# Kernel optimization log

Hardware: AMD Instinct MI355X
Metric: run time of the kernel (lower is better)

The kernel has to match this reference:

```python
import jax, jax.numpy as jnp
import numpy as np

N, M, D = 8192, 8192, 512
TINY = jnp.finfo(jnp.float32).tiny


def setup_inputs() -> dict:
    key = jax.random.key(0)
    k1, k2 = jax.random.split(key)
    x = jax.random.normal(k1, (N, D), dtype=jnp.float32)
    x2 = jax.random.normal(k2, (M, D), dtype=jnp.float32)
    # flax self.param with ones initializer (pre-softplus raw params)
    amplitude_raw = jnp.ones((1,), dtype=jnp.float32)
    length_scale_raw = jnp.ones((D,), dtype=jnp.float32)
    return {"x": x, "x2": x2, "amplitude_raw": amplitude_raw,
            "length_scale_raw": length_scale_raw}


def reference(x, x2, amplitude_raw, length_scale_raw):
    # Parameter transforms exactly as in RBFKernelProvider.apply
    amplitude = jax.nn.softplus(amplitude_raw) + TINY          # (1,)
    length_scale = jax.nn.softplus(length_scale_raw) + TINY    # (D,)

    # rbf_kernel_fun: exp(-0.5 * sum(((x - x2)/l)^2)) * amp^2
    # GEMM rewrite of the squared scaled distance (avoids (N,M,D) intermediate):
    # ||xs_i - ys_j||^2 = ||xs_i||^2 + ||ys_j||^2 - 2 xs_i . ys_j
    xs = x / length_scale                                       # (N, D)
    ys = x2 / length_scale                                      # (M, D)
    x_sq = jnp.sum(xs * xs, axis=-1)                            # (N,)
    y_sq = jnp.sum(ys * ys, axis=-1)                            # (M,)
    cross = jnp.einsum('nd,md->nm', xs, ys)                     # (N, M) GEMM
    sq_dists = jnp.maximum(x_sq[:, None] + y_sq[None, :] - 2.0 * cross, 0.0)
    kernel_matrix = jnp.exp(-0.5 * sq_dists)                    # (N, M)
    return (amplitude ** 2) * kernel_matrix
```

## Files before the change

kernel.cpp:

```cpp
#include <hip/hip_runtime.h>

#define AS1 __attribute__((address_space(1)))
#define AS3 __attribute__((address_space(3)))

typedef __attribute__((ext_vector_type(4))) float f32x4;
typedef __attribute__((ext_vector_type(8))) int   i32x8;

static constexpr int Nn = 8192;
static constexpr int Mm = 8192;
static constexpr int Dd = 512;
static constexpr float TINY = 1.17549435082228751e-38f;

__device__ __forceinline__ float softplus_f(float x) {
    return fmaxf(x, 0.0f) + log1pf(expf(-fabsf(x)));
}

__device__ __forceinline__ float fast_exp2(float x) {
#if __has_builtin(__builtin_amdgcn_exp2f)
    return __builtin_amdgcn_exp2f(x);
#else
    return exp2f(x);
#endif
}

__device__ __forceinline__ void g2l16(const void* g, void* l) {
    __builtin_amdgcn_global_load_lds((const AS1 unsigned int*)g,
                                     (AS3 unsigned int*)l, 16, 0, 0);
}

__global__ __launch_bounds__(256) void scale_rows(
        const float* __restrict__ x, const float* __restrict__ x2,
        const float* __restrict__ ls_raw,
        unsigned char* __restrict__ xs, unsigned char* __restrict__ ys,
        float* __restrict__ x_sq, float* __restrict__ y_sq) {
    int wave = threadIdx.x >> 6, lane = threadIdx.x & 63;
    int row = blockIdx.x * 4 + wave;

    const float* src; unsigned char* dst; float* nrm; int r;
    if (row < Nn) {
        src = x  + (size_t)row * Dd; dst = xs + (size_t)row * 512;
        nrm = x_sq + row; r = row;
    } else {
        int m = row - Nn;
        src = x2 + (size_t)m * Dd;   dst = ys + (size_t)m * 512;
        nrm = y_sq + m; r = m;
    }

    float4 v0 = ((const float4*)src)[lane * 2];
    float4 v1 = ((const float4*)src)[lane * 2 + 1];
    float4 L0 = ((const float4*)ls_raw)[lane * 2];
    float4 L1 = ((const float4*)ls_raw)[lane * 2 + 1];

    float il[8] = {
        1.0f / (softplus_f(L0.x) + TINY), 1.0f / (softplus_f(L0.y) + TINY),
        1.0f / (softplus_f(L0.z) + TINY), 1.0f / (softplus_f(L0.w) + TINY),
        1.0f / (softplus_f(L1.x) + TINY), 1.0f / (softplus_f(L1.y) + TINY),
        1.0f / (softplus_f(L1.z) + TINY), 1.0f / (softplus_f(L1.w) + TINY) };
    float s[8] = { v0.x*il[0], v0.y*il[1], v0.z*il[2], v0.w*il[3],
                   v1.x*il[4], v1.y*il[5], v1.z*il[6], v1.w*il[7] };
    float sum = 0.0f;
#pragma unroll
    for (int i = 0; i < 8; ++i) sum += s[i] * s[i];

    int p0 = __builtin_amdgcn_cvt_pk_fp8_f32(s[0], s[1], 0, false);
    p0     = __builtin_amdgcn_cvt_pk_fp8_f32(s[2], s[3], p0, true);
    int p1 = __builtin_amdgcn_cvt_pk_fp8_f32(s[4], s[5], 0, false);
    p1     = __builtin_amdgcn_cvt_pk_fp8_f32(s[6], s[7], p1, true);

    int j    = lane >> 1;
    int phys = (j & ~7) | ((j & 7) ^ (r & 7));
    *(int2*)(dst + phys * 16 + (lane & 1) * 8) = make_int2(p0, p1);

#pragma unroll
    for (int off = 32; off > 0; off >>= 1) sum += __shfl_down(sum, off, 64);
    if (lane == 0) *nrm = sum;
}

__global__ __launch_bounds__(256) void gemm_rbf(
        const unsigned char* __restrict__ xs,
        const unsigned char* __restrict__ ys,
        const float* __restrict__ x_sq, const float* __restrict__ y_sq,
        const float* __restrict__ amp_raw, float* __restrict__ out) {

    __shared__ unsigned char smem[32768];
    unsigned char* sA = smem;
    unsigned char* sB = smem + 16384;
    float* sT = (float*)smem;

    const int tid  = threadIdx.x;
    const int wave = tid >> 6, lane = tid & 63;
    const int wy = wave >> 1, wx = wave & 1;
    const int lane15 = lane & 15, quad = lane >> 4;
    const int srow = lane >> 3, schunk = lane & 7;

    const unsigned lin = blockIdx.y * 64u + blockIdx.x;
    const unsigned swz = (lin & 7u) * 512u + (lin >> 3);
    const size_t rowBase = (size_t)(swz >> 6) * 128;
    const size_t colBase = (size_t)(swz & 63u) * 128;

    float xq[4][4], yq[4];
#pragma unroll
    for (int ty = 0; ty < 4; ++ty) {
        const size_t r0 = rowBase + wy * 64 + ty * 16 + quad * 4;
#pragma unroll
        for (int i = 0; i < 4; ++i) xq[ty][i] = x_sq[r0 + i];
    }
#pragma unroll
    for (int tx = 0; tx < 4; ++tx)
        yq[tx] = y_sq[colBase + wx * 64 + tx * 16 + lane15];
    float a = softplus_f(amp_raw[0]) + TINY;

    f32x4 acc[4][4] = {};

    for (int kt = 0; kt < 4; ++kt) {
        __syncthreads();
        const size_t kOff = (size_t)kt * 128;
#pragma unroll
        for (int t = 0; t < 4; ++t) {
            int issue = wave * 4 + t;
            int rit = issue * 8 + srow;
            g2l16(xs + (rowBase + rit) * 512 + kOff + schunk * 16,
                  sA + issue * 1024);
            g2l16(ys + (colBase + rit) * 512 + kOff + schunk * 16,
                  sB + issue * 1024);
        }
        __syncthreads();

        i32x8 bF[4];
#pragma unroll
        for (int tx = 0; tx < 4; ++tx) {
            int rr = wx * 64 + tx * 16 + lane15;
            int x7 = rr & 7;
            int p0 = (quad * 2 + 0) ^ x7, p1 = (quad * 2 + 1) ^ x7;
            int4 lo = *(const int4*)(sB + rr * 128 + p0 * 16);
            int4 hi = *(const int4*)(sB + rr * 128 + p1 * 16);
            i32x8 f; f[0]=lo.x; f[1]=lo.y; f[2]=lo.z; f[3]=lo.w;
                     f[4]=hi.x; f[5]=hi.y; f[6]=hi.z; f[7]=hi.w;
            bF[tx] = f;
        }
#pragma unroll
        for (int ty = 0; ty < 4; ++ty) {
            int rr = wy * 64 + ty * 16 + lane15;
            int x7 = rr & 7;
            int p0 = (quad * 2 + 0) ^ x7, p1 = (quad * 2 + 1) ^ x7;
            int4 lo = *(const int4*)(sA + rr * 128 + p0 * 16);
            int4 hi = *(const int4*)(sA + rr * 128 + p1 * 16);
            i32x8 aF; aF[0]=lo.x; aF[1]=lo.y; aF[2]=lo.z; aF[3]=lo.w;
                      aF[4]=hi.x; aF[5]=hi.y; aF[6]=hi.z; aF[7]=hi.w;
#pragma unroll
            for (int tx = 0; tx < 4; ++tx)
                acc[ty][tx] = __builtin_amdgcn_mfma_scale_f32_16x16x128_f8f6f4(
                    aF, bF[tx], acc[ty][tx],
                    0 , 0 ,
                    0, 0x7F7F7F7F,
                    0, 0x7F7F7F7F);
        }
    }

    const float L2E = 1.44269504088896340736f;
    const float la  = 2.0f * __log2f(a);
    float hx[4][4], hy[4];
#pragma unroll
    for (int ty = 0; ty < 4; ++ty)
#pragma unroll
        for (int i = 0; i < 4; ++i) hx[ty][i] = -0.5f * L2E * xq[ty][i];
#pragma unroll
    for (int tx = 0; tx < 4; ++tx) hy[tx] = -0.5f * L2E * yq[tx];

    __syncthreads();
#pragma unroll
    for (int ty = 0; ty < 4; ++ty) {
#pragma unroll
        for (int tx = 0; tx < 4; ++tx) {
#pragma unroll
            for (int reg = 0; reg < 4; ++reg) {
                float t = fminf(fmaf(acc[ty][tx][reg], L2E,
                                     hx[ty][reg] + hy[tx]), 0.0f);
                sT[(wy * 16 + quad * 4 + reg) * 132 +
                   (wx * 64 + tx * 16 + lane15)] = fast_exp2(t + la);
            }
        }
        __syncthreads();
#pragma unroll
        for (int i = 0; i < 4; ++i) {
            int l    = wave * 8 + i * 2 + (lane >> 5);
            int grow = (l >> 4) * 64 + ty * 16 + (l & 15);
            int col  = (lane & 31) * 4;
            f32x4 v  = *(const f32x4*)(sT + l * 132 + col);
            __builtin_nontemporal_store(v,
                (f32x4*)(out + (rowBase + grow) * (size_t)Mm + colBase + col));
        }
        __syncthreads();
    }
}

__global__ __launch_bounds__(256) void rbf_fallback(
        const float* __restrict__ x, const float* __restrict__ x2,
        const float* __restrict__ amp_raw, const float* __restrict__ ls_raw,
        float* __restrict__ out) {
    __shared__ float il[Dd];
    __shared__ float sX[16 * Dd];
    __shared__ float sY[16 * Dd];
    int tid = threadIdx.x;
    for (int i = tid; i < Dd; i += 256)
        il[i] = 1.0f / (softplus_f(ls_raw[i]) + TINY);
    __syncthreads();
    int bR = blockIdx.y * 16, bC = blockIdx.x * 16;
    for (int i = tid; i < 16 * Dd; i += 256) {
        int r = i >> 9, c = i & (Dd - 1);
        sX[i] = x [(size_t)(bR + r) * Dd + c] * il[c];
        sY[i] = x2[(size_t)(bC + r) * Dd + c] * il[c];
    }
    __syncthreads();
    float a = softplus_f(amp_raw[0]) + TINY;
    float amp2 = a * a;
    int r = tid >> 4, c = tid & 15;
    float sq = 0.0f;
    for (int d = 0; d < Dd; ++d) {
        float df = sX[r * Dd + d] - sY[c * Dd + d];
        sq += df * df;
    }
    out[(size_t)(bR + r) * Mm + (bC + c)] = amp2 * __expf(-0.5f * sq);
}

extern "C" void kernel_launch(void* const* d_in, const int* in_sizes, int n_in,
                              void* d_out, int out_size, void* d_ws, size_t ws_size,
                              hipStream_t stream) {
    const float* x       = (const float*)d_in[0];
    const float* x2      = (const float*)d_in[1];
    const float* amp_raw = (const float*)d_in[2];
    const float* ls_raw  = (const float*)d_in[3];
    float* out = (float*)d_out;

    const size_t OFF_XSQ = 0;
    const size_t OFF_YSQ = OFF_XSQ + 8192 * 4;
    const size_t OFF_XS  = OFF_YSQ + 8192 * 4;
    const size_t OFF_YS  = OFF_XS + (size_t)Nn * Dd;
    const size_t NEED    = OFF_YS + (size_t)Mm * Dd;

    if (ws_size < NEED) {
        dim3 g(Mm / 16, Nn / 16);
        rbf_fallback<<<g, 256, 0, stream>>>(x, x2, amp_raw, ls_raw, out);
        return;
    }

    char* ws = (char*)d_ws;
    float* x_sq = (float*)(ws + OFF_XSQ);
    float* y_sq = (float*)(ws + OFF_YSQ);
    unsigned char* xs = (unsigned char*)(ws + OFF_XS);
    unsigned char* ys = (unsigned char*)(ws + OFF_YS);

    scale_rows<<<(Nn + Mm) / 4, 256, 0, stream>>>(x, x2, ls_raw, xs, ys, x_sq, y_sq);
    dim3 g(Mm / 128, Nn / 128);
    gemm_rbf<<<g, 256, 0, stream>>>(xs, ys, x_sq, y_sq, amp_raw, out);
}
```

Before: 331.3 us.

## Double-buffer FP8 GEMM K-tiles in LDS with explicit vmcnt waits

Doubles shared memory to 64 KB so the FP8 A/B K-tiles can be double-buffered. The global-to-LDS load for the next K step is issued before the MFMA work on the current tile, with explicit s_waitcnt vmcnt and s_barrier calls in place of __syncthreads. This is meant to hide global load latency behind matrix compute. The larger LDS footprint can reduce how many blocks fit per CU, and the hand-written vmcnt counts must match the number of outstanding loads.

```diff
diff --git a/kernel.cpp b/kernel.cpp
--- a/kernel.cpp
+++ b/kernel.cpp
@@ -82,9 +82,9 @@
         const float* __restrict__ x_sq, const float* __restrict__ y_sq,
         const float* __restrict__ amp_raw, float* __restrict__ out) {
 
-    __shared__ unsigned char smem[32768];
-    unsigned char* sA = smem;
-    unsigned char* sB = smem + 16384;
+    __shared__ unsigned char smem[65536];
+    unsigned char* sAb[2] = { smem,         smem + 16384 };
+    unsigned char* sBb[2] = { smem + 32768, smem + 49152 };
     float* sT = (float*)smem;
 
     const int tid  = threadIdx.x;
@@ -98,34 +98,36 @@
     const size_t rowBase = (size_t)(swz >> 6) * 128;
     const size_t colBase = (size_t)(swz & 63u) * 128;
 
-    float xq[4][4], yq[4];
-#pragma unroll
-    for (int ty = 0; ty < 4; ++ty) {
-        const size_t r0 = rowBase + wy * 64 + ty * 16 + quad * 4;
-#pragma unroll
-        for (int i = 0; i < 4; ++i) xq[ty][i] = x_sq[r0 + i];
-    }
-#pragma unroll
-    for (int tx = 0; tx < 4; ++tx)
-        yq[tx] = y_sq[colBase + wx * 64 + tx * 16 + lane15];
-    float a = softplus_f(amp_raw[0]) + TINY;
-
-    f32x4 acc[4][4] = {};
-
-    for (int kt = 0; kt < 4; ++kt) {
-        __syncthreads();
+    auto stage = [&](int buf, int kt) {
         const size_t kOff = (size_t)kt * 128;
 #pragma unroll
         for (int t = 0; t < 4; ++t) {
             int issue = wave * 4 + t;
             int rit = issue * 8 + srow;
             g2l16(xs + (rowBase + rit) * 512 + kOff + schunk * 16,
-                  sA + issue * 1024);
+                  sAb[buf] + issue * 1024);
             g2l16(ys + (colBase + rit) * 512 + kOff + schunk * 16,
-                  sB + issue * 1024);
-        }
-        __syncthreads();
-
+                  sBb[buf] + issue * 1024);
+        }
+    };
+
+    float xq[4][4], yq[4];
+#pragma unroll
+    for (int ty = 0; ty < 4; ++ty) {
+        const size_t r0 = rowBase + wy * 64 + ty * 16 + quad * 4;
+#pragma unroll
+        for (int i = 0; i < 4; ++i) xq[ty][i] = x_sq[r0 + i];
+    }
+#pragma unroll
+    for (int tx = 0; tx < 4; ++tx)
+        yq[tx] = y_sq[colBase + wx * 64 + tx * 16 + lane15];
+    float a = softplus_f(amp_raw[0]) + TINY;
+
+    f32x4 acc[4][4] = {};
+
+    auto compute = [&](int buf) {
+        const unsigned char* sA = sAb[buf];
+        const unsigned char* sB = sBb[buf];
         i32x8 bF[4];
 #pragma unroll
         for (int tx = 0; tx < 4; ++tx) {
@@ -155,7 +157,23 @@
                     0, 0x7F7F7F7F,
                     0, 0x7F7F7F7F);
         }
-    }
+    };
+
+    stage(0, 0);
+#define KSTEP(KT, PREFETCH, VM)                                         \
+    {                                                                   \
+        if (PREFETCH) stage(((KT) + 1) & 1, (KT) + 1);                  \
+        asm volatile("s_waitcnt vmcnt(" VM ")" ::: "memory");           \
+        __builtin_amdgcn_s_barrier();                                   \
+        __builtin_amdgcn_sched_barrier(0);                              \
+        compute((KT) & 1);                                              \
+        __builtin_amdgcn_s_barrier();                                   \
+    }
+    KSTEP(0, 1, "8")
+    KSTEP(1, 1, "8")
+    KSTEP(2, 1, "8")
+    KSTEP(3, 0, "0")
+#undef KSTEP
 
     const float L2E = 1.44269504088896340736f;
     const float la  = 2.0f * __log2f(a);
@@ -167,7 +185,6 @@
 #pragma unroll
     for (int tx = 0; tx < 4; ++tx) hy[tx] = -0.5f * L2E * yq[tx];
 
-    __syncthreads();
 #pragma unroll
     for (int ty = 0; ty < 4; ++ty) {
 #pragma unroll
```

Measured after the change: 326.7 us. No clear change (-1.4%).
